# Performance work log

Measured on AMD Instinct MI355X. Metric: run time of the kernel, lower is better.

Reference implementation:

```python
import jax, jax.numpy as jnp
import numpy as np

B = 4096
IN_F = 4096
OUT_F = 4096
IN_Q = IN_F // 4
OUT_Q = OUT_F // 4


def setup_inputs() -> dict:
    key = jax.random.key(0)
    ks = jax.random.split(key, 9)
    scale = 1.0 / np.sqrt(IN_Q)
    inp = {"x": jax.random.normal(ks[0], (B, IN_F), dtype=jnp.float32)}
    for i, name in enumerate(["rr", "ri", "rj", "rk"]):
        inp[f"W_{name}"] = jax.random.uniform(ks[1 + i], (OUT_Q, IN_Q), dtype=jnp.float32, minval=-scale, maxval=scale)
        inp[f"b_{name}"] = jax.random.uniform(ks[5 + i], (OUT_Q,), dtype=jnp.float32, minval=-scale, maxval=scale)
    return inp


def reference(x, W_rr, W_ri, W_rj, W_rk, b_rr, b_ri, b_rj, b_rk):
    b = x.shape[0]
    # split into quaternion components: chunks c in {r,i,j,k}
    xs = x.reshape(b, 4, IN_Q)                       # [B, 4, IN_Q]
    W = jnp.stack([W_rr, W_ri, W_rj, W_rk])          # [4(lin), OUT_Q, IN_Q]
    bias = jnp.stack([b_rr, b_ri, b_rj, b_rk])       # [4(lin), OUT_Q]
    # all 16 linear applications in one batched GEMM: Y[b,c,q,:] = lin_q(x_c)
    Y = jnp.einsum('bci,qoi->bcqo', xs, W) + bias    # [B, 4, 4, OUT_Q]
    out_r = Y[:, 0, 0] - Y[:, 1, 1] - Y[:, 2, 2] - Y[:, 3, 3]
    out_i = Y[:, 0, 1] + Y[:, 1, 0] + Y[:, 2, 3] - Y[:, 3, 2]
    out_j = Y[:, 0, 2] - Y[:, 1, 3] + Y[:, 2, 0] + Y[:, 3, 1]
    out_k = Y[:, 0, 3] + Y[:, 1, 2] - Y[:, 2, 1] + Y[:, 3, 0]
    out = jnp.stack([out_r, out_i, out_j, out_k], axis=1)  # [B, 4, OUT_Q]
    return out.reshape(b, -1)                        # [B, OUT_F]
```

## Files before the change

kernel.cpp:

```cpp
#include <hip/hip_runtime.h>
#include <cstdint>
#include <cstddef>

#define MDIM 4096
#define NDIM 4096
#define KDIM 4096

typedef _Float16 half8   __attribute__((ext_vector_type(8)));
typedef float    floatx4 __attribute__((ext_vector_type(4)));

__device__ __constant__ int   d_qtab[16] = {0,1,2,3,  1,0,3,2,  2,3,0,1,  3,2,1,0};
__device__ __constant__ float d_stab[16] = {1.f,-1.f,-1.f,-1.f,
                                            1.f, 1.f, 1.f,-1.f,
                                            1.f,-1.f, 1.f, 1.f,
                                            1.f, 1.f,-1.f, 1.f};

__global__ void prepass_kernel(const float* __restrict__ x,
                               const float* __restrict__ W0, const float* __restrict__ W1,
                               const float* __restrict__ W2, const float* __restrict__ W3,
                               _Float16* __restrict__ xh, _Float16* __restrict__ Wh) {
    int b = blockIdx.x;
    if (b < 8192) {
        int idx = b * 256 + threadIdx.x;
        const float4* src = (const float4*)x + (size_t)idx * 2;
        float4 a = src[0], v = src[1];
        half8 h = {(_Float16)a.x, (_Float16)a.y, (_Float16)a.z, (_Float16)a.w,
                   (_Float16)v.x, (_Float16)v.y, (_Float16)v.z, (_Float16)v.w};
        ((half8*)xh)[idx] = h;
    } else {
        int idx = (b - 8192) * 256 + threadIdx.x;
        int e = idx << 3;
        int m = e >> 20;
        int off = e & ((1 << 20) - 1);
        const float* Ws[4] = {W0, W1, W2, W3};
        const float* src = Ws[m] + off;
        float4 a = *(const float4*)src;
        float4 v = *(const float4*)(src + 4);
        half8 h = {(_Float16)a.x, (_Float16)a.y, (_Float16)a.z, (_Float16)a.w,
                   (_Float16)v.x, (_Float16)v.y, (_Float16)v.z, (_Float16)v.w};
        *(half8*)(Wh + ((size_t)m << 20) + off) = h;
    }
}


__device__ __forceinline__ void gload_lds16(const _Float16* g, _Float16* l) {
    __builtin_amdgcn_global_load_lds(
        (const __attribute__((address_space(1))) unsigned int*)g,
        (__attribute__((address_space(3))) unsigned int*)l,
        16, 0, 0);
}

#define BAR __builtin_amdgcn_s_barrier()
#define SCHEDB __builtin_amdgcn_sched_barrier(0)
#define WAITVM(N) asm volatile("s_waitcnt vmcnt(" #N ")" ::: "memory")

#define STA(g, tt, buf) { \
    const _Float16* _s = Abase + (size_t)((g) * 64) * KDIM + (tt) * 64; \
    _Float16* _d = AsSt + (buf) * 16384 + (g) * 8192; \
    gload_lds16(_s, _d); \
    gload_lds16(_s + (size_t)128 * KDIM, _d + 4096); }

#define STB(h, tt, buf) { \
    const int _sg = (tt) >> 4; \
    const _Float16* _s = Bbase + ((size_t)(comp ^ _sg) << 20) \
                       + (size_t)((h) * 128) * 1024 + ((tt) & 15) * 64; \
    _Float16* _d = BsSt + (buf) * 16384 + (h) * 8192; \
    gload_lds16(_s, _d); \
    gload_lds16(_s + 64 * 1024, _d + 4096); }

#define RDA(AF, BASE, g, SL) { \
    const _Float16* _p = (BASE) + (g) * 8192 + arow + (SL); \
    AF[0] = *(const half8*)(_p); \
    AF[1] = *(const half8*)(_p + 1024); \
    AF[2] = *(const half8*)(_p + 2048); \
    AF[3] = *(const half8*)(_p + 3072); }

#define RDB(BQ, BASE, SL, NEG) { \
    const _Float16* _p = (BASE) + bnh * 8192 + brow + (SL); \
    BQ[0] = *(const half8*)(_p); \
    BQ[1] = *(const half8*)(_p + 1024); \
    BQ[2] = *(const half8*)(_p + 2048); \
    BQ[3] = *(const half8*)(_p + 3072); \
    if (NEG) { BQ[0] = -BQ[0]; BQ[1] = -BQ[1]; BQ[2] = -BQ[2]; BQ[3] = -BQ[3]; } }

#define MFMA16(IB, AF, BQ) \
    _Pragma("unroll") \
    for (int _i = 0; _i < 4; _i++) \
      _Pragma("unroll") \
      for (int _j = 0; _j < 4; _j++) \
        acc[(IB) + _i][_j] = __builtin_amdgcn_mfma_f32_16x16x32_f16( \
            AF[_i], BQ[_j], acc[(IB) + _i][_j], 0, 0, 0);

__global__ __launch_bounds__(512, 2) void gemm_kernel(
        const _Float16* __restrict__ A,
        const _Float16* __restrict__ Wh,
        const float* __restrict__ b0, const float* __restrict__ b1,
        const float* __restrict__ b2, const float* __restrict__ b3,
        float* __restrict__ C) {
    __shared__ _Float16 lds[65536];
    _Float16* As = lds;
    _Float16* Bs = lds + 32768;

    const int tid  = threadIdx.x;
    const int lane = tid & 63;
    const int wave = tid >> 6;
    const int wmh  = wave >> 2;
    const int wn   = (wave & 3) * 64;
    const int bnh  = wn >> 7;
    const int broff = (wn & 64) * 64;

    const int wg = ((blockIdx.x & 7) << 5) | (blockIdx.x >> 3);
    const int bm = wg >> 4, bn = wg & 15;
    const int m0 = bm << 8;
    const int n0 = bn << 8;
    const int comp = bn >> 2;
    const int n0q  = n0 & 1023;

    const int lrow = tid >> 3;
    const int gch  = (tid & 7) ^ (lrow & 7);
    const _Float16* Abase = A  + (size_t)(m0  + lrow) * KDIM + gch * 8;
    const _Float16* Bbase = Wh + (size_t)(n0q + lrow) * 1024 + gch * 8;
    _Float16* AsSt = As + tid * 8;
    _Float16* BsSt = Bs + tid * 8;

    const int fr  = lane & 15;
    const int qf  = lane >> 4;
    const int fsw = fr & 7;
    const int sl0 = ((0 + qf) ^ fsw) * 8;
    const int sl1 = ((4 + qf) ^ fsw) * 8;
    const int arow = wmh * 4096 + fr * 64;
    const int brow = broff + fr * 64;

    const int negseg = (comp == 0) ? 0 : (comp == 1) ? 3 : (comp == 2) ? 1 : 2;
    const float flip = (comp == 0) ? -1.f : 1.f;

    floatx4 acc[8][4];
#pragma unroll
    for (int i = 0; i < 8; i++)
#pragma unroll
        for (int j = 0; j < 4; j++)
            acc[i][j] = (floatx4){0.f, 0.f, 0.f, 0.f};

    half8 afP[4], afQ[4], bf0[4], bf1[4];

    STA(0, 0, 0); STB(0, 0, 0); STB(1, 0, 0); STA(1, 0, 0);
    STA(0, 1, 1); STB(0, 1, 1);
    WAITVM(6);
    BAR;
    RDA(afP, As, 0, sl0); RDB(bf0, Bs, sl0, (0 == negseg));

    for (int tt = 0; tt < 64; ++tt) {
        const int cur = tt & 1, nxt = cur ^ 1;
        const bool bneg  = ((tt >> 4) == negseg);
        const _Float16* Acur = As + cur * 16384;
        const _Float16* Bcur = Bs + cur * 16384;
        const _Float16* Anxt = As + nxt * 16384;
        const _Float16* Bnxt = Bs + nxt * 16384;
        const int t1 = (tt >= 63) ? 63 : tt + 1;
        const int t2 = (tt >= 62) ? 63 : tt + 2;
        const bool bneg1 = ((t1 >> 4) == negseg);

        RDA(afQ, Acur, 0, sl1); RDB(bf1, Bcur, sl1, bneg);
        STB(1, t1, nxt);
        SCHEDB;
        __builtin_amdgcn_s_setprio(1);
        MFMA16(0, afP, bf0);
        __builtin_amdgcn_s_setprio(0);
        WAITVM(6);
        BAR;

        RDA(afP, Acur, 1, sl0);
        STA(1, t1, nxt);
        SCHEDB;
        __builtin_amdgcn_s_setprio(1);
        MFMA16(0, afQ, bf1);
        __builtin_amdgcn_s_setprio(0);
        BAR;

        RDA(afQ, Acur, 1, sl1);
        STA(0, t2, cur);
        SCHEDB;
        __builtin_amdgcn_s_setprio(1);
        MFMA16(4, afP, bf0);
        __builtin_amdgcn_s_setprio(0);
        WAITVM(4);
        BAR;

        RDA(afP, Anxt, 0, sl0); RDB(bf0, Bnxt, sl0, bneg1);
        STB(0, t2, cur);
        SCHEDB;
        __builtin_amdgcn_s_setprio(1);
        MFMA16(4, afQ, bf1);
        __builtin_amdgcn_s_setprio(0);
        BAR;
    }

    WAITVM(0);

    const int col   = lane & 15;
    const int rquad = (lane >> 4) * 4;
    const int wm    = wmh * 128;
    const float* bsp[4] = {b0, b1, b2, b3};
#pragma unroll
    for (int j = 0; j < 4; j++) {
        const int gn = n0 + wn + j * 16 + col;
        const int o  = gn & 1023;
        float bv = 0.f;
#pragma unroll
        for (int c = 0; c < 4; c++)
            bv += d_stab[comp * 4 + c] * bsp[comp ^ c][o];
#pragma unroll
        for (int i = 0; i < 8; i++) {
            const int gmb = m0 + wm + i * 16 + rquad;
#pragma unroll
            for (int r = 0; r < 4; r++)
                C[(size_t)(gmb + r) * NDIM + gn] = flip * acc[i][j][r] + bv;
        }
    }
}

__global__ void fallback_kernel(const float* __restrict__ x,
                                const float* __restrict__ W0, const float* __restrict__ W1,
                                const float* __restrict__ W2, const float* __restrict__ W3,
                                const float* __restrict__ b0, const float* __restrict__ b1,
                                const float* __restrict__ b2, const float* __restrict__ b3,
                                float* __restrict__ out) {
    int idx = blockIdx.x * 256 + threadIdx.x;
    int m = idx >> 12, n = idx & 4095;
    int comp = n >> 10, o = n & 1023;
    const float* Ws[4] = {W0, W1, W2, W3};
    const float* bs[4] = {b0, b1, b2, b3};
    float acc = 0.f;
    for (int c = 0; c < 4; c++) {
        int t = comp * 4 + c;
        const float* wr = Ws[d_qtab[t]] + (size_t)o * 1024;
        const float* xr = x + (size_t)m * 4096 + c * 1024;
        float s = d_stab[t];
        float dot = 0.f;
        for (int i = 0; i < 1024; i += 4) {
            float4 wv = *(const float4*)(wr + i);
            float4 xv = *(const float4*)(xr + i);
            dot += wv.x * xv.x + wv.y * xv.y + wv.z * xv.z + wv.w * xv.w;
        }
        acc += s * dot + s * bs[d_qtab[t]][o];
    }
    out[idx] = acc;
}

extern "C" void kernel_launch(void* const* d_in, const int* in_sizes, int n_in,
                              void* d_out, int out_size, void* d_ws, size_t ws_size,
                              hipStream_t stream) {
    const float* x = (const float*)d_in[0];
    const float* W[4];
    const float* b[4];
    int wi = 0, bi = 0;
    for (int i = 1; i < n_in && i < 9; i++) {
        if (in_sizes[i] > 4096) { if (wi < 4) W[wi++] = (const float*)d_in[i]; }
        else                    { if (bi < 4) b[bi++] = (const float*)d_in[i]; }
    }
    float* out = (float*)d_out;

    const size_t xh_elems = (size_t)MDIM * KDIM;
    const size_t wh_elems = (size_t)4 * 1024 * 1024;
    const size_t needed = (xh_elems + wh_elems) * 2;

    if (ws_size < needed) {
        fallback_kernel<<<(MDIM * NDIM) / 256, 256, 0, stream>>>(
            x, W[0], W[1], W[2], W[3], b[0], b[1], b[2], b[3], out);
        return;
    }

    _Float16* xh = (_Float16*)d_ws;
    _Float16* Wh = xh + xh_elems;

    prepass_kernel<<<8192 + 2048, 256, 0, stream>>>(x, W[0], W[1], W[2], W[3], xh, Wh);
    gemm_kernel<<<(MDIM / 256) * (NDIM / 256), 512, 0, stream>>>(
        xh, Wh, b[0], b[1], b[2], b[3], out);
}
```

Baseline: 257.1 us.

## Load weight fragments directly from global into registers, bypassing LDS

Stops staging the weight tile in shared memory. Each wave now loads its B fragments straight from global memory into registers, which halves the kernel's LDS footprint. The per-segment negation of B fragments is replaced by negating the accumulators at segment boundaries, with a matching sign applied in the epilogue. The cost is strided, less coalesced global loads on the MFMA critical path and vmcnt waits that may now also cover the register loads.

```diff
diff --git a/kernel.cpp b/kernel.cpp
--- a/kernel.cpp
+++ b/kernel.cpp
@@ -60,13 +60,13 @@
     gload_lds16(_s, _d); \
     gload_lds16(_s + (size_t)128 * KDIM, _d + 4096); }
 
-#define STB(h, tt, buf) { \
-    const int _sg = (tt) >> 4; \
-    const _Float16* _s = Bbase + ((size_t)(comp ^ _sg) << 20) \
-                       + (size_t)((h) * 128) * 1024 + ((tt) & 15) * 64; \
-    _Float16* _d = BsSt + (buf) * 16384 + (h) * 8192; \
-    gload_lds16(_s, _d); \
-    gload_lds16(_s + 64 * 1024, _d + 4096); }
+#define LDB(BQ, TT, KH) { \
+    const _Float16* _bp = Wh + ((size_t)(comp ^ ((TT) >> 4)) << 20) \
+                             + ((TT) & 15) * 64 + (KH) * 32; \
+    BQ[0] = *(const half8*)(_bp + boff0); \
+    BQ[1] = *(const half8*)(_bp + boff1); \
+    BQ[2] = *(const half8*)(_bp + boff2); \
+    BQ[3] = *(const half8*)(_bp + boff3); }
 
 #define RDA(AF, BASE, g, SL) { \
     const _Float16* _p = (BASE) + (g) * 8192 + arow + (SL); \
@@ -74,14 +74,6 @@
     AF[1] = *(const half8*)(_p + 1024); \
     AF[2] = *(const half8*)(_p + 2048); \
     AF[3] = *(const half8*)(_p + 3072); }
-
-#define RDB(BQ, BASE, SL, NEG) { \
-    const _Float16* _p = (BASE) + bnh * 8192 + brow + (SL); \
-    BQ[0] = *(const half8*)(_p); \
-    BQ[1] = *(const half8*)(_p + 1024); \
-    BQ[2] = *(const half8*)(_p + 2048); \
-    BQ[3] = *(const half8*)(_p + 3072); \
-    if (NEG) { BQ[0] = -BQ[0]; BQ[1] = -BQ[1]; BQ[2] = -BQ[2]; BQ[3] = -BQ[3]; } }
 
 #define MFMA16(IB, AF, BQ) \
     _Pragma("unroll") \
@@ -97,17 +89,14 @@
         const float* __restrict__ b0, const float* __restrict__ b1,
         const float* __restrict__ b2, const float* __restrict__ b3,
         float* __restrict__ C) {
-    __shared__ _Float16 lds[65536];
+    __shared__ _Float16 lds[32768];
     _Float16* As = lds;
-    _Float16* Bs = lds + 32768;
 
     const int tid  = threadIdx.x;
     const int lane = tid & 63;
     const int wave = tid >> 6;
     const int wmh  = wave >> 2;
     const int wn   = (wave & 3) * 64;
-    const int bnh  = wn >> 7;
-    const int broff = (wn & 64) * 64;
 
     const int wg = ((blockIdx.x & 7) << 5) | (blockIdx.x >> 3);
     const int bm = wg >> 4, bn = wg & 15;
@@ -118,10 +107,8 @@
 
     const int lrow = tid >> 3;
     const int gch  = (tid & 7) ^ (lrow & 7);
-    const _Float16* Abase = A  + (size_t)(m0  + lrow) * KDIM + gch * 8;
-    const _Float16* Bbase = Wh + (size_t)(n0q + lrow) * 1024 + gch * 8;
+    const _Float16* Abase = A + (size_t)(m0 + lrow) * KDIM + gch * 8;
     _Float16* AsSt = As + tid * 8;
-    _Float16* BsSt = Bs + tid * 8;
 
     const int fr  = lane & 15;
     const int qf  = lane >> 4;
@@ -129,10 +116,17 @@
     const int sl0 = ((0 + qf) ^ fsw) * 8;
     const int sl1 = ((4 + qf) ^ fsw) * 8;
     const int arow = wmh * 4096 + fr * 64;
-    const int brow = broff + fr * 64;
+
+    const int brow_g = n0q + wn + fr;
+    const int boff0 = (brow_g +  0) * 1024 + qf * 8;
+    const int boff1 = (brow_g + 16) * 1024 + qf * 8;
+    const int boff2 = (brow_g + 32) * 1024 + qf * 8;
+    const int boff3 = (brow_g + 48) * 1024 + qf * 8;
 
     const int negseg = (comp == 0) ? 0 : (comp == 1) ? 3 : (comp == 2) ? 1 : 2;
-    const float flip = (comp == 0) ? -1.f : 1.f;
+    const int negFlipA = (negseg == 0) ? 16 : negseg * 16;
+    const int negFlipB = (negseg == 0 || negseg == 3) ? -1 : negseg * 16 + 16;
+    const float esign = (comp <= 1) ? -1.f : 1.f;
 
     floatx4 acc[8][4];
 #pragma unroll
@@ -143,34 +137,38 @@
 
     half8 afP[4], afQ[4], bf0[4], bf1[4];
 
-    STA(0, 0, 0); STB(0, 0, 0); STB(1, 0, 0); STA(1, 0, 0);
-    STA(0, 1, 1); STB(0, 1, 1);
+    STA(0, 0, 0); STA(1, 0, 0);
+    STA(0, 1, 1);
+    LDB(bf0, 0, 0);
     WAITVM(6);
     BAR;
-    RDA(afP, As, 0, sl0); RDB(bf0, Bs, sl0, (0 == negseg));
+    RDA(afP, As, 0, sl0);
 
     for (int tt = 0; tt < 64; ++tt) {
         const int cur = tt & 1, nxt = cur ^ 1;
-        const bool bneg  = ((tt >> 4) == negseg);
         const _Float16* Acur = As + cur * 16384;
-        const _Float16* Bcur = Bs + cur * 16384;
         const _Float16* Anxt = As + nxt * 16384;
-        const _Float16* Bnxt = Bs + nxt * 16384;
         const int t1 = (tt >= 63) ? 63 : tt + 1;
         const int t2 = (tt >= 62) ? 63 : tt + 2;
-        const bool bneg1 = ((t1 >> 4) == negseg);
-
-        RDA(afQ, Acur, 0, sl1); RDB(bf1, Bcur, sl1, bneg);
-        STB(1, t1, nxt);
+
+        if (tt == negFlipA || tt == negFlipB) {
+#pragma unroll
+            for (int i = 0; i < 8; i++)
+#pragma unroll
+                for (int j = 0; j < 4; j++)
+                    acc[i][j] = -acc[i][j];
+        }
+
+        RDA(afQ, Acur, 0, sl1);
+        LDB(bf1, tt, 1);
+        STA(1, t1, nxt);
         SCHEDB;
         __builtin_amdgcn_s_setprio(1);
         MFMA16(0, afP, bf0);
         __builtin_amdgcn_s_setprio(0);
-        WAITVM(6);
         BAR;
 
         RDA(afP, Acur, 1, sl0);
-        STA(1, t1, nxt);
         SCHEDB;
         __builtin_amdgcn_s_setprio(1);
         MFMA16(0, afQ, bf1);
@@ -183,15 +181,15 @@
         __builtin_amdgcn_s_setprio(1);
         MFMA16(4, afP, bf0);
         __builtin_amdgcn_s_setprio(0);
-        WAITVM(4);
-        BAR;
-
-        RDA(afP, Anxt, 0, sl0); RDB(bf0, Bnxt, sl0, bneg1);
-        STB(0, t2, cur);
+        BAR;
+
+        RDA(afP, Anxt, 0, sl0);
+        LDB(bf0, t1, 0);
         SCHEDB;
         __builtin_amdgcn_s_setprio(1);
         MFMA16(4, afQ, bf1);
         __builtin_amdgcn_s_setprio(0);
+        WAITVM(6);
         BAR;
     }
 
@@ -214,7 +212,7 @@
             const int gmb = m0 + wm + i * 16 + rquad;
 #pragma unroll
             for (int r = 0; r < 4; r++)
-                C[(size_t)(gmb + r) * NDIM + gn] = flip * acc[i][j][r] + bv;
+                C[(size_t)(gmb + r) * NDIM + gn] = esign * acc[i][j][r] + bv;
         }
     }
 }
```

Measured after the change: 329.5 us. +28.2%, slower.

## Fuse fp32-to-fp16 activation conversion into GEMM A-tile loads

Applied to the files above, without the earlier changes.

Drops the separate x conversion pass. The GEMM now loads fp32 activations into registers, converts them to fp16 and writes them to LDS itself, replacing async global-to-LDS loads for A. This avoids writing and re-reading a 32MB fp16 copy of x. Per-fragment B negation is replaced by flipping the sign of the accumulator at segment boundaries, and the pipeline is restructured into four phases with explicit lgkm waits. The cost is twice the A global traffic per tile and synchronous register staging, which may hurt load/compute overlap.

```diff
diff --git a/kernel.cpp b/kernel.cpp
--- a/kernel.cpp
+++ b/kernel.cpp
@@ -15,31 +15,20 @@
                                             1.f,-1.f, 1.f, 1.f,
                                             1.f, 1.f,-1.f, 1.f};
 
-__global__ void prepass_kernel(const float* __restrict__ x,
-                               const float* __restrict__ W0, const float* __restrict__ W1,
+__global__ void prepass_kernel(const float* __restrict__ W0, const float* __restrict__ W1,
                                const float* __restrict__ W2, const float* __restrict__ W3,
-                               _Float16* __restrict__ xh, _Float16* __restrict__ Wh) {
-    int b = blockIdx.x;
-    if (b < 8192) {
-        int idx = b * 256 + threadIdx.x;
-        const float4* src = (const float4*)x + (size_t)idx * 2;
-        float4 a = src[0], v = src[1];
-        half8 h = {(_Float16)a.x, (_Float16)a.y, (_Float16)a.z, (_Float16)a.w,
-                   (_Float16)v.x, (_Float16)v.y, (_Float16)v.z, (_Float16)v.w};
-        ((half8*)xh)[idx] = h;
-    } else {
-        int idx = (b - 8192) * 256 + threadIdx.x;
-        int e = idx << 3;
-        int m = e >> 20;
-        int off = e & ((1 << 20) - 1);
-        const float* Ws[4] = {W0, W1, W2, W3};
-        const float* src = Ws[m] + off;
-        float4 a = *(const float4*)src;
-        float4 v = *(const float4*)(src + 4);
-        half8 h = {(_Float16)a.x, (_Float16)a.y, (_Float16)a.z, (_Float16)a.w,
-                   (_Float16)v.x, (_Float16)v.y, (_Float16)v.z, (_Float16)v.w};
-        *(half8*)(Wh + ((size_t)m << 20) + off) = h;
-    }
+                               _Float16* __restrict__ Wh) {
+    int idx = blockIdx.x * 256 + threadIdx.x;
+    int e = idx << 3;
+    int m = e >> 20;
+    int off = e & ((1 << 20) - 1);
+    const float* Ws[4] = {W0, W1, W2, W3};
+    const float* src = Ws[m] + off;
+    float4 a = *(const float4*)src;
+    float4 v = *(const float4*)(src + 4);
+    half8 h = {(_Float16)a.x, (_Float16)a.y, (_Float16)a.z, (_Float16)a.w,
+               (_Float16)v.x, (_Float16)v.y, (_Float16)v.z, (_Float16)v.w};
+    *(half8*)(Wh + ((size_t)m << 20) + off) = h;
 }
 
 
@@ -53,12 +42,31 @@
 #define BAR __builtin_amdgcn_s_barrier()
 #define SCHEDB __builtin_amdgcn_sched_barrier(0)
 #define WAITVM(N) asm volatile("s_waitcnt vmcnt(" #N ")" ::: "memory")
-
-#define STA(g, tt, buf) { \
-    const _Float16* _s = Abase + (size_t)((g) * 64) * KDIM + (tt) * 64; \
-    _Float16* _d = AsSt + (buf) * 16384 + (g) * 8192; \
-    gload_lds16(_s, _d); \
-    gload_lds16(_s + (size_t)128 * KDIM, _d + 4096); }
+#define WAITLGKM0 do { asm volatile("s_waitcnt lgkmcnt(0)" ::: "memory"); \
+                       SCHEDB; } while (0)
+
+#define AISSUE(TT) { \
+    const float* _a = Xbase + (TT) * 64; \
+    aS0 = *(const float4*)(_a);                      \
+    aS1 = *(const float4*)(_a + 4);                  \
+    aS2 = *(const float4*)(_a + (size_t)128 * 4096); \
+    aS3 = *(const float4*)(_a + (size_t)128 * 4096 + 4); \
+    aS4 = *(const float4*)(_a + (size_t)64 * 4096);  \
+    aS5 = *(const float4*)(_a + (size_t)64 * 4096 + 4); \
+    aS6 = *(const float4*)(_a + (size_t)192 * 4096); \
+    aS7 = *(const float4*)(_a + (size_t)192 * 4096 + 4); }
+
+__device__ __forceinline__ half8 cvt8(float4 a, float4 b) {
+    return (half8){(_Float16)a.x, (_Float16)a.y, (_Float16)a.z, (_Float16)a.w,
+                   (_Float16)b.x, (_Float16)b.y, (_Float16)b.z, (_Float16)b.w};
+}
+
+#define CVTWR(BUF) { \
+    _Float16* _d = AsSt + (BUF) * 16384; \
+    *(half8*)(_d)         = cvt8(aS0, aS1); \
+    *(half8*)(_d +  4096) = cvt8(aS2, aS3); \
+    *(half8*)(_d +  8192) = cvt8(aS4, aS5); \
+    *(half8*)(_d + 12288) = cvt8(aS6, aS7); }
 
 #define STB(h, tt, buf) { \
     const int _sg = (tt) >> 4; \
@@ -75,13 +83,12 @@
     AF[2] = *(const half8*)(_p + 2048); \
     AF[3] = *(const half8*)(_p + 3072); }
 
-#define RDB(BQ, BASE, SL, NEG) { \
+#define RDB(BQ, BASE, SL) { \
     const _Float16* _p = (BASE) + bnh * 8192 + brow + (SL); \
     BQ[0] = *(const half8*)(_p); \
     BQ[1] = *(const half8*)(_p + 1024); \
     BQ[2] = *(const half8*)(_p + 2048); \
-    BQ[3] = *(const half8*)(_p + 3072); \
-    if (NEG) { BQ[0] = -BQ[0]; BQ[1] = -BQ[1]; BQ[2] = -BQ[2]; BQ[3] = -BQ[3]; } }
+    BQ[3] = *(const half8*)(_p + 3072); }
 
 #define MFMA16(IB, AF, BQ) \
     _Pragma("unroll") \
@@ -92,7 +99,7 @@
             AF[_i], BQ[_j], acc[(IB) + _i][_j], 0, 0, 0);
 
 __global__ __launch_bounds__(512, 2) void gemm_kernel(
-        const _Float16* __restrict__ A,
+        const float* __restrict__ X,
         const _Float16* __restrict__ Wh,
         const float* __restrict__ b0, const float* __restrict__ b1,
         const float* __restrict__ b2, const float* __restrict__ b3,
@@ -118,7 +125,7 @@
 
     const int lrow = tid >> 3;
     const int gch  = (tid & 7) ^ (lrow & 7);
-    const _Float16* Abase = A  + (size_t)(m0  + lrow) * KDIM + gch * 8;
+    const float*    Xbase = X  + (size_t)(m0  + lrow) * 4096 + gch * 8;
     const _Float16* Bbase = Wh + (size_t)(n0q + lrow) * 1024 + gch * 8;
     _Float16* AsSt = As + tid * 8;
     _Float16* BsSt = Bs + tid * 8;
@@ -132,7 +139,9 @@
     const int brow = broff + fr * 64;
 
     const int negseg = (comp == 0) ? 0 : (comp == 1) ? 3 : (comp == 2) ? 1 : 2;
-    const float flip = (comp == 0) ? -1.f : 1.f;
+    const int negFlipA = (negseg == 0) ? 16 : negseg * 16;
+    const int negFlipB = (negseg == 0 || negseg == 3) ? -1 : negseg * 16 + 16;
+    const float esign = (comp <= 1) ? -1.f : 1.f;
 
     floatx4 acc[8][4];
 #pragma unroll
@@ -141,61 +150,67 @@
         for (int j = 0; j < 4; j++)
             acc[i][j] = (floatx4){0.f, 0.f, 0.f, 0.f};
 
-    half8 afP[4], afQ[4], bf0[4], bf1[4];
-
-    STA(0, 0, 0); STB(0, 0, 0); STB(1, 0, 0); STA(1, 0, 0);
-    STA(0, 1, 1); STB(0, 1, 1);
-    WAITVM(6);
+    half8 af[4], bf0[4], bf1[4];
+    float4 aS0, aS1, aS2, aS3, aS4, aS5, aS6, aS7;
+
+    AISSUE(0);
+    STB(0, 0, 0); STB(1, 0, 0);
+    WAITVM(4);
+    CVTWR(0);
+    asm volatile("s_waitcnt lgkmcnt(0)" ::: "memory");
+    WAITVM(0);
     BAR;
-    RDA(afP, As, 0, sl0); RDB(bf0, Bs, sl0, (0 == negseg));
 
     for (int tt = 0; tt < 64; ++tt) {
         const int cur = tt & 1, nxt = cur ^ 1;
-        const bool bneg  = ((tt >> 4) == negseg);
         const _Float16* Acur = As + cur * 16384;
         const _Float16* Bcur = Bs + cur * 16384;
-        const _Float16* Anxt = As + nxt * 16384;
-        const _Float16* Bnxt = Bs + nxt * 16384;
         const int t1 = (tt >= 63) ? 63 : tt + 1;
-        const int t2 = (tt >= 62) ? 63 : tt + 2;
-        const bool bneg1 = ((t1 >> 4) == negseg);
-
-        RDA(afQ, Acur, 0, sl1); RDB(bf1, Bcur, sl1, bneg);
+
+        if (tt == negFlipA || tt == negFlipB) {
+#pragma unroll
+            for (int i = 0; i < 8; i++)
+#pragma unroll
+                for (int j = 0; j < 4; j++)
+                    acc[i][j] = -acc[i][j];
+        }
+
+        RDA(af, Acur, 0, sl0);
+        RDB(bf0, Bcur, sl0);
+        AISSUE(t1);
+        WAITLGKM0;
+        __builtin_amdgcn_s_setprio(1);
+        MFMA16(0, af, bf0);
+        __builtin_amdgcn_s_setprio(0);
+        BAR;
+
+        RDA(af, Acur, 0, sl1);
+        RDB(bf1, Bcur, sl1);
+        STB(0, t1, nxt);
         STB(1, t1, nxt);
-        SCHEDB;
-        __builtin_amdgcn_s_setprio(1);
-        MFMA16(0, afP, bf0);
-        __builtin_amdgcn_s_setprio(0);
-        WAITVM(6);
-        BAR;
-
-        RDA(afP, Acur, 1, sl0);
-        STA(1, t1, nxt);
-        SCHEDB;
-        __builtin_amdgcn_s_setprio(1);
-        MFMA16(0, afQ, bf1);
-        __builtin_amdgcn_s_setprio(0);
-        BAR;
-
-        RDA(afQ, Acur, 1, sl1);
-        STA(0, t2, cur);
-        SCHEDB;
-        __builtin_amdgcn_s_setprio(1);
-        MFMA16(4, afP, bf0);
-        __builtin_amdgcn_s_setprio(0);
+        WAITLGKM0;
+        __builtin_amdgcn_s_setprio(1);
+        MFMA16(0, af, bf1);
+        __builtin_amdgcn_s_setprio(0);
+        BAR;
+
+        RDA(af, Acur, 1, sl0);
         WAITVM(4);
-        BAR;
-
-        RDA(afP, Anxt, 0, sl0); RDB(bf0, Bnxt, sl0, bneg1);
-        STB(0, t2, cur);
-        SCHEDB;
-        __builtin_amdgcn_s_setprio(1);
-        MFMA16(4, afQ, bf1);
-        __builtin_amdgcn_s_setprio(0);
-        BAR;
-    }
-
-    WAITVM(0);
+        CVTWR(nxt);
+        WAITLGKM0;
+        __builtin_amdgcn_s_setprio(1);
+        MFMA16(4, af, bf0);
+        __builtin_amdgcn_s_setprio(0);
+        BAR;
+
+        RDA(af, Acur, 1, sl1);
+        WAITLGKM0;
+        __builtin_amdgcn_s_setprio(1);
+        MFMA16(4, af, bf1);
+        __builtin_amdgcn_s_setprio(0);
+        WAITVM(0);
+        BAR;
+    }
 
     const int col   = lane & 15;
     const int rquad = (lane >> 4) * 4;
@@ -214,7 +229,7 @@
             const int gmb = m0 + wm + i * 16 + rquad;
 #pragma unroll
             for (int r = 0; r < 4; r++)
-                C[(size_t)(gmb + r) * NDIM + gn] = flip * acc[i][j][r] + bv;
+                C[(size_t)(gmb + r) * NDIM + gn] = esign * acc[i][j][r] + bv;
         }
     }
 }
@@ -260,9 +275,8 @@
     }
     float* out = (float*)d_out;
 
-    const size_t xh_elems = (size_t)MDIM * KDIM;
     const size_t wh_elems = (size_t)4 * 1024 * 1024;
-    const size_t needed = (xh_elems + wh_elems) * 2;
+    const size_t needed = wh_elems * 2;
 
     if (ws_size < needed) {
         fallback_kernel<<<(MDIM * NDIM) / 256, 256, 0, stream>>>(
@@ -270,10 +284,9 @@
         return;
     }
 
-    _Float16* xh = (_Float16*)d_ws;
-    _Float16* Wh = xh + xh_elems;
-
-    prepass_kernel<<<8192 + 2048, 256, 0, stream>>>(x, W[0], W[1], W[2], W[3], xh, Wh);
+    _Float16* Wh = (_Float16*)d_ws;
+
+    prepass_kernel<<<2048, 256, 0, stream>>>(W[0], W[1], W[2], W[3], Wh);
     gemm_kernel<<<(MDIM / 256) * (NDIM / 256), 512, 0, stream>>>(
-        xh, Wh, b[0], b[1], b[2], b[3], out);
-}
+        x, Wh, b[0], b[1], b[2], b[3], out);
+}
```

Result: slower. 304.6 us (+18.5%).
